# Performance work log

Hardware: AMD Instinct MI355X
Metric: run time of the kernel (lower is better)

## Reference

```python
import jax, jax.numpy as jnp
import numpy as np

N = 8192          # total nodes in the batch of graphs
ATOM = 64         # atom_feats
HID = 128         # hidden_feats
HEADS = 8         # num_heads
NUM_GRAPHS = 256  # number of graphs (max value of `batch`)
NEG_SLOPE = 0.2   # LeakyReLU slope in GAT attention


def setup_inputs() -> dict:
    key = jax.random.key(0)
    ks = jax.random.split(key, 16)
    x = jax.random.normal(ks[0], (N, ATOM), dtype=jnp.float32)
    adj = (jax.random.uniform(ks[1], (N, N)) < 0.01).astype(jnp.float32)
    adj = jnp.maximum(adj, jnp.eye(N, dtype=jnp.float32))
    batch = jnp.sort(jax.random.randint(ks[2], (N,), 0, NUM_GRAPHS)).astype(jnp.int32)

    def u(k, shape, fan_in):
        lim = 1.0 / np.sqrt(fan_in)
        return jax.random.uniform(k, shape, jnp.float32, -lim, lim)

    in1 = HID * HEADS
    params = dict(
        W0=u(ks[3], (ATOM, HID), ATOM), a0_src=u(ks[4], (HID,), HID), a0_dst=u(ks[5], (HID,), HID),
        W1=u(ks[6], (in1, HID), in1), a1_src=u(ks[7], (HID,), HID), a1_dst=u(ks[8], (HID,), HID),
        W2=u(ks[9], (in1, HID), in1), a2_src=u(ks[10], (HID,), HID), a2_dst=u(ks[11], (HID,), HID),
        fc_w=u(ks[12], (HID, 1), HID), fc_b=u(ks[13], (1,), HID),
    )
    return dict(x=x, adj=adj, batch=batch, **params)


def _gat_layer(h_in, W, a_src, a_dst, mask):
    # standard dense GAT: Wh, e_ij = leakyrelu(a_src.Wh_i + a_dst.Wh_j), masked softmax, aggregate
    h = h_in @ W                                         # [N, HID]
    e = jax.nn.leaky_relu((h @ a_src)[:, None] + (h @ a_dst)[None, :], NEG_SLOPE)  # [N, N]
    e = jnp.where(mask, e, jnp.float32(-1e9))
    attn = jax.nn.softmax(e, axis=1)                     # [N, N]
    return attn @ h                                      # [N, HID]


def reference(x, adj, batch, W0, a0_src, a0_dst, W1, a1_src, a1_dst, W2, a2_src, a2_dst, fc_w, fc_b):
    # eval mode: dropout is identity. The torch module calls the SAME layer instance per head,
    # so concat of heads == tile, and the final stacked mean == a single layer call.
    mask = adj > 0
    h0 = _gat_layer(x, W0, a0_src, a0_dst, mask)
    x1 = jax.nn.relu(jnp.tile(h0, (1, HEADS)))           # [N, HID*HEADS]
    h1 = _gat_layer(x1, W1, a1_src, a1_dst, mask)
    x2 = jax.nn.relu(jnp.tile(h1, (1, HEADS)))
    h2 = _gat_layer(x2, W2, a2_src, a2_dst, mask)        # mean over identical heads == h2
    # global mean pool over graphs
    sums = jax.ops.segment_sum(h2, batch, num_segments=NUM_GRAPHS)           # [G, HID]
    cnt = jax.ops.segment_sum(jnp.ones((N, 1), h2.dtype), batch, num_segments=NUM_GRAPHS)
    pooled = sums / jnp.maximum(cnt, 1.0)
    out = pooled @ fc_w + fc_b                           # [G, 1]
    return out[:, 0]
```

## Files before the change

### kernel.cpp

```cpp
#include <hip/hip_runtime.h>
#include <cstdint>
#include <cstddef>

#define NN 8192
#define ATOMF 64
#define HID 128
#define HEADS 8
#define NG 256
#define ELLW 192
#define NEGSLOPE 0.2f

typedef unsigned long long u64;

__global__ __launch_bounds__(256, 4) void k_scan_ell(const float* __restrict__ adj,
                                                     int* __restrict__ ell,
                                                     int* __restrict__ deg) {
    __shared__ u64 bml[4][128];
    int t = threadIdx.x, wid = t >> 6, l = t & 63;
    int row = blockIdx.x * 4 + wid;
    const float4* a4 = (const float4*)(adj + (size_t)row * NN);
    u64* bmr = bml[wid];
    #pragma unroll 8
    for (int s = 0; s < 32; ++s) {
        float4 v = a4[s * 64 + l];
        u64 b0 = __ballot(v.x > 0.f);
        u64 b1 = __ballot(v.y > 0.f);
        u64 b2 = __ballot(v.z > 0.f);
        u64 b3 = __ballot(v.w > 0.f);
        if (l < 4) bmr[s * 4 + l] = (l == 0) ? b0 : (l == 1) ? b1 : (l == 2) ? b2 : b3;
    }
    __syncthreads();
    u64 w0 = bmr[2 * l];
    u64 w1 = bmr[2 * l + 1];
    int c = __popcll(w0) + __popcll(w1);
    int incl = c;
    #pragma unroll
    for (int o = 1; o < 64; o <<= 1) {
        int u = __shfl_up(incl, o);
        if (l >= o) incl += u;
    }
    int pos = incl - c;
    int total = __shfl(incl, 63);
    if (l == 0) deg[row] = total < ELLW ? total : ELLW;
    int* er = ell + (size_t)row * ELLW;
    int gw0 = 2 * l, gw1 = 2 * l + 1;
    int base0 = (gw0 >> 2) * 256 + (gw0 & 3);
    int base1 = (gw1 >> 2) * 256 + (gw1 & 3);
    while (w0) {
        int bit = __builtin_ctzll(w0);
        w0 &= w0 - 1;
        if (pos < ELLW) er[pos++] = base0 + 4 * bit;
    }
    while (w1) {
        int bit = __builtin_ctzll(w1);
        w1 &= w1 - 1;
        if (pos < ELLW) er[pos++] = base1 + 4 * bit;
    }
}

__global__ __launch_bounds__(256) void k_front2(
    const float* __restrict__ x,
    const float* __restrict__ W0, const float* __restrict__ a0s, const float* __restrict__ a0d,
    const float* __restrict__ W1, const float* __restrict__ W2,
    float* __restrict__ Wr1, float* __restrict__ Wr2,
    float* __restrict__ g0, float* __restrict__ ssrc, float* __restrict__ sdst) {
    int b = blockIdx.x, t = threadIdx.x;
    if (b < 128) {
        const float* W = (b < 64) ? W1 : W2;
        float* Wr = (b < 64) ? Wr1 : Wr2;
        int i = (b & 63) * 256 + t;
        int k = i >> 7, cc = i & 127;
        float s = 0.f;
        #pragma unroll
        for (int h = 0; h < HEADS; ++h) s += W[(size_t)(h * HID + k) * HID + cc];
        Wr[i] = s;
    } else {
        __shared__ float Xl[32 * ATOMF];
        int row0 = (b - 128) * 32;
        const float4* Xg = (const float4*)(x + (size_t)row0 * ATOMF);
        float4* Xl4 = (float4*)Xl;
        #pragma unroll
        for (int i = t; i < 32 * ATOMF / 4; i += 256) Xl4[i] = Xg[i];
        __syncthreads();
        int cg = t & 31, rg = t >> 5;
        int c0 = cg * 4;
        float acc[4][4];
        #pragma unroll
        for (int r = 0; r < 4; ++r)
            #pragma unroll
            for (int c = 0; c < 4; ++c) acc[r][c] = 0.f;
        for (int k = 0; k < ATOMF; k += 4) {
            float4 w0 = *(const float4*)(W0 + (size_t)(k + 0) * HID + c0);
            float4 w1 = *(const float4*)(W0 + (size_t)(k + 1) * HID + c0);
            float4 w2 = *(const float4*)(W0 + (size_t)(k + 2) * HID + c0);
            float4 w3 = *(const float4*)(W0 + (size_t)(k + 3) * HID + c0);
            #pragma unroll
            for (int r = 0; r < 4; ++r) {
                float4 xv = *(const float4*)(&Xl[(rg * 4 + r) * ATOMF + k]);
                acc[r][0] += xv.x * w0.x + xv.y * w1.x + xv.z * w2.x + xv.w * w3.x;
                acc[r][1] += xv.x * w0.y + xv.y * w1.y + xv.z * w2.y + xv.w * w3.y;
                acc[r][2] += xv.x * w0.z + xv.y * w1.z + xv.z * w2.z + xv.w * w3.z;
                acc[r][3] += xv.x * w0.w + xv.y * w1.w + xv.z * w2.w + xv.w * w3.w;
            }
        }
        float4 asv = *(const float4*)(a0s + c0);
        float4 adv = *(const float4*)(a0d + c0);
        #pragma unroll
        for (int r = 0; r < 4; ++r) {
            int row = row0 + rg * 4 + r;
            *(float4*)(g0 + (size_t)row * HID + c0) =
                make_float4(acc[r][0], acc[r][1], acc[r][2], acc[r][3]);
            float ps = acc[r][0] * asv.x + acc[r][1] * asv.y + acc[r][2] * asv.z + acc[r][3] * asv.w;
            float pd = acc[r][0] * adv.x + acc[r][1] * adv.y + acc[r][2] * adv.z + acc[r][3] * adv.w;
            #pragma unroll
            for (int o = 16; o; o >>= 1) {
                ps += __shfl_xor(ps, o);
                pd += __shfl_xor(pd, o);
            }
            if (cg == 0) { ssrc[row] = ps; sdst[row] = pd; }
        }
    }
}

template<int DO_GEMM>
__global__ __launch_bounds__(256, 4) void k_layer(
    const float* __restrict__ g, const float* __restrict__ ssrc_in,
    const float* __restrict__ sdst_in,
    const int* __restrict__ ell, const int* __restrict__ deg,
    const float* __restrict__ Wr, const float* __restrict__ as_,
    const float* __restrict__ ad_,
    float* __restrict__ gout, float* __restrict__ ssrc_out,
    float* __restrict__ sdst_out) {
    __shared__ float wls[4][ELLW + 2];
    __shared__ int jls[4][ELLW + 2];
    __shared__ float xls[4][HID];
    int wid = threadIdx.x >> 6, l = threadIdx.x & 63;
    int row = blockIdx.x * 4 + wid;
    float* wl = wls[wid];
    int* jl = jls[wid];
    int d = deg[row];
    float si = ssrc_in[row];
    const int* er = ell + (size_t)row * ELLW;
    float m = -1e30f;
    for (int k = l; k < d; k += 64) {
        int j = er[k];
        float e = si + sdst_in[j];
        e = e > 0.f ? e : NEGSLOPE * e;
        jl[k] = j << 7;
        wl[k] = e;
        m = fmaxf(m, e);
    }
    #pragma unroll
    for (int o = 32; o; o >>= 1) m = fmaxf(m, __shfl_xor(m, o));
    float s = 0.f;
    for (int k = l; k < d; k += 64) {
        float w = __expf(wl[k] - m);
        wl[k] = w;
        s += w;
    }
    #pragma unroll
    for (int o = 32; o; o >>= 1) s += __shfl_xor(s, o);
    float inv = 1.f / s;
    if ((d & 1) && l == 0) { wl[d] = 0.f; jl[d] = 0; }
    int dpad = d + (d & 1);
    int half = l >> 5;
    int d0 = (l & 31) * 4;
    const float* hd = g + d0;
    float4 acc = make_float4(0.f, 0.f, 0.f, 0.f);
    int k = 0;
    for (; k + 8 <= dpad; k += 8) {
        int j0 = jl[k + half],     j1 = jl[k + 2 + half];
        int j2 = jl[k + 4 + half], j3 = jl[k + 6 + half];
        float w0 = wl[k + half],     w1 = wl[k + 2 + half];
        float w2 = wl[k + 4 + half], w3 = wl[k + 6 + half];
        float4 v0 = *(const float4*)(hd + j0);
        float4 v1 = *(const float4*)(hd + j1);
        float4 v2 = *(const float4*)(hd + j2);
        float4 v3 = *(const float4*)(hd + j3);
        acc.x += w0 * v0.x; acc.y += w0 * v0.y; acc.z += w0 * v0.z; acc.w += w0 * v0.w;
        acc.x += w1 * v1.x; acc.y += w1 * v1.y; acc.z += w1 * v1.z; acc.w += w1 * v1.w;
        acc.x += w2 * v2.x; acc.y += w2 * v2.y; acc.z += w2 * v2.z; acc.w += w2 * v2.w;
        acc.x += w3 * v3.x; acc.y += w3 * v3.y; acc.z += w3 * v3.z; acc.w += w3 * v3.w;
    }
    for (; k < dpad; k += 2) {
        int j = jl[k + half];
        float w = wl[k + half];
        float4 v = *(const float4*)(hd + j);
        acc.x += w * v.x; acc.y += w * v.y; acc.z += w * v.z; acc.w += w * v.w;
    }
    acc.x += __shfl_xor(acc.x, 32);
    acc.y += __shfl_xor(acc.y, 32);
    acc.z += __shfl_xor(acc.z, 32);
    acc.w += __shfl_xor(acc.w, 32);
    acc.x *= inv; acc.y *= inv; acc.z *= inv; acc.w *= inv;
    if (DO_GEMM == 0) {
        if (l < 32)
            *(float4*)(gout + (size_t)row * HID + d0) = acc;
        return;
    }
    float* xl = xls[wid];
    if (l < 32) {
        float4 r;
        r.x = fmaxf(acc.x, 0.f); r.y = fmaxf(acc.y, 0.f);
        r.z = fmaxf(acc.z, 0.f); r.w = fmaxf(acc.w, 0.f);
        *(float4*)(xl + d0) = r;
    }
    float acc0 = 0.f, acc1 = 0.f;
    for (int kk = 0; kk < HID; kk += 4) {
        float4 xv = *(const float4*)(&xl[kk]);
        float wa0 = Wr[(size_t)(kk + 0) * HID + l];
        float wb0 = Wr[(size_t)(kk + 0) * HID + l + 64];
        float wa1 = Wr[(size_t)(kk + 1) * HID + l];
        float wb1 = Wr[(size_t)(kk + 1) * HID + l + 64];
        float wa2 = Wr[(size_t)(kk + 2) * HID + l];
        float wb2 = Wr[(size_t)(kk + 2) * HID + l + 64];
        float wa3 = Wr[(size_t)(kk + 3) * HID + l];
        float wb3 = Wr[(size_t)(kk + 3) * HID + l + 64];
        acc0 += xv.x * wa0 + xv.y * wa1 + xv.z * wa2 + xv.w * wa3;
        acc1 += xv.x * wb0 + xv.y * wb1 + xv.z * wb2 + xv.w * wb3;
    }
    gout[(size_t)row * HID + l]      = acc0;
    gout[(size_t)row * HID + l + 64] = acc1;
    float ps = acc0 * as_[l] + acc1 * as_[l + 64];
    float pd = acc0 * ad_[l] + acc1 * ad_[l + 64];
    #pragma unroll
    for (int o = 32; o; o >>= 1) {
        ps += __shfl_xor(ps, o);
        pd += __shfl_xor(pd, o);
    }
    if (l == 0) { ssrc_out[row] = ps; sdst_out[row] = pd; }
}

__global__ __launch_bounds__(256) void k_poolfc(const float* __restrict__ h,
                                                const int* __restrict__ batch,
                                                const float* __restrict__ fcw,
                                                const float* __restrict__ fcb,
                                                float* __restrict__ out) {
    int wid = threadIdx.x >> 6, l = threadIdx.x & 63;
    int g = blockIdx.x * 4 + wid;
    int lo = 0, hi = NN;
    while (lo < hi) { int mid = (lo + hi) >> 1; if (batch[mid] < g) lo = mid + 1; else hi = mid; }
    int e0 = lo;
    hi = NN;
    while (lo < hi) { int mid = (lo + hi) >> 1; if (batch[mid] <= g) lo = mid + 1; else hi = mid; }
    int e1 = lo;
    float sum = 0.f;
    for (int r = e0; r < e1; ++r) {
        const float* hr = h + (size_t)r * HID;
        sum += hr[l] * fcw[l] + hr[l + 64] * fcw[l + 64];
    }
    #pragma unroll
    for (int o = 32; o; o >>= 1) sum += __shfl_xor(sum, o);
    if (l == 0) out[g] = sum / fmaxf((float)(e1 - e0), 1.f) + fcb[0];
}

extern "C" void kernel_launch(void* const* d_in, const int* in_sizes, int n_in,
                              void* d_out, int out_size, void* d_ws, size_t ws_size,
                              hipStream_t stream) {
    const float* x    = (const float*)d_in[0];
    const float* adj  = (const float*)d_in[1];
    const int*   batch= (const int*)  d_in[2];
    const float* W0   = (const float*)d_in[3];
    const float* a0s  = (const float*)d_in[4];
    const float* a0d  = (const float*)d_in[5];
    const float* W1   = (const float*)d_in[6];
    const float* a1s  = (const float*)d_in[7];
    const float* a1d  = (const float*)d_in[8];
    const float* W2   = (const float*)d_in[9];
    const float* a2s  = (const float*)d_in[10];
    const float* a2d  = (const float*)d_in[11];
    const float* fcw  = (const float*)d_in[12];
    const float* fcb  = (const float*)d_in[13];
    float* out = (float*)d_out;

    char* ws = (char*)d_ws;
    size_t off = 0;
    auto alloc = [&](size_t bytes) {
        char* p = ws + off;
        off = (off + bytes + 255) & ~255UL;
        return p;
    };
    int*   ell  = (int*)  alloc((size_t)NN * ELLW * 4);
    int*   deg  = (int*)  alloc((size_t)NN * 4);
    float* hA   = (float*)alloc((size_t)NN * HID * 4);
    float* hB   = (float*)alloc((size_t)NN * HID * 4);
    float* sAs  = (float*)alloc((size_t)NN * 4);
    float* sAd  = (float*)alloc((size_t)NN * 4);
    float* sBs  = (float*)alloc((size_t)NN * 4);
    float* sBd  = (float*)alloc((size_t)NN * 4);
    float* Wr1  = (float*)alloc((size_t)HID * HID * 4);
    float* Wr2  = (float*)alloc((size_t)HID * HID * 4);
    (void)ws_size; (void)in_sizes; (void)n_in; (void)out_size;

    k_scan_ell<<<NN / 4, 256, 0, stream>>>(adj, ell, deg);
    k_front2<<<128 + 256, 256, 0, stream>>>(x, W0, a0s, a0d, W1, W2,
                                            Wr1, Wr2, hA, sAs, sAd);
    k_layer<1><<<NN / 4, 256, 0, stream>>>(hA, sAs, sAd, ell, deg, Wr1, a1s, a1d,
                                           hB, sBs, sBd);
    k_layer<1><<<NN / 4, 256, 0, stream>>>(hB, sBs, sBd, ell, deg, Wr2, a2s, a2d,
                                           hA, sAs, sAd);
    k_layer<0><<<NN / 4, 256, 0, stream>>>(hA, sAs, sAd, ell, deg, nullptr, nullptr,
                                           nullptr, hB, nullptr, nullptr);
    k_poolfc<<<NG / 4, 256, 0, stream>>>(hB, batch, fcw, fcb, out);
}
```

Before: 171.1 us.

## Store node features in fp16 and drop softmax max-subtraction pass

Intermediate node feature matrices are now stored as fp16 to halve the bytes moved by the neighbor gather in each GAT layer. The per-row max reduction before the exponent is removed, so exp is computed directly in one pass. Degree is stored in an int4 record, and the GEMM weight loads are vectorised as float2. These changes risk lost precision and overflow in exp for large logits, but the main runtime is dominated by the adjacency scan, which is unchanged.

```diff
diff --git a/kernel.cpp b/kernel.cpp
--- a/kernel.cpp
+++ b/kernel.cpp
@@ -1,4 +1,5 @@
 #include <hip/hip_runtime.h>
+#include <hip/hip_fp16.h>
 #include <cstdint>
 #include <cstddef>
 
@@ -14,7 +15,7 @@
 
 __global__ __launch_bounds__(256, 4) void k_scan_ell(const float* __restrict__ adj,
                                                      int* __restrict__ ell,
-                                                     int* __restrict__ deg) {
+                                                     int4* __restrict__ tb) {
     __shared__ u64 bml[4][128];
     int t = threadIdx.x, wid = t >> 6, l = t & 63;
     int row = blockIdx.x * 4 + wid;
@@ -41,7 +42,12 @@
     }
     int pos = incl - c;
     int total = __shfl(incl, 63);
-    if (l == 0) deg[row] = total < ELLW ? total : ELLW;
+    if (l == 0) {
+        int4 b;
+        b.x = b.y = b.z = 0;
+        b.w = total < ELLW ? total : ELLW;
+        tb[row] = b;
+    }
     int* er = ell + (size_t)row * ELLW;
     int gw0 = 2 * l, gw1 = 2 * l + 1;
     int base0 = (gw0 >> 2) * 256 + (gw0 & 3);
@@ -63,7 +69,7 @@
     const float* __restrict__ W0, const float* __restrict__ a0s, const float* __restrict__ a0d,
     const float* __restrict__ W1, const float* __restrict__ W2,
     float* __restrict__ Wr1, float* __restrict__ Wr2,
-    float* __restrict__ g0, float* __restrict__ ssrc, float* __restrict__ sdst) {
+    __half* __restrict__ g016, float* __restrict__ ssrc, float* __restrict__ sdst) {
     int b = blockIdx.x, t = threadIdx.x;
     if (b < 128) {
         const float* W = (b < 64) ? W1 : W2;
@@ -108,8 +114,10 @@
         #pragma unroll
         for (int r = 0; r < 4; ++r) {
             int row = row0 + rg * 4 + r;
-            *(float4*)(g0 + (size_t)row * HID + c0) =
-                make_float4(acc[r][0], acc[r][1], acc[r][2], acc[r][3]);
+            __half2 p0 = __floats2half2_rn(acc[r][0], acc[r][1]);
+            __half2 p1 = __floats2half2_rn(acc[r][2], acc[r][3]);
+            __half2* gp = (__half2*)(g016 + (size_t)row * HID + c0);
+            gp[0] = p0; gp[1] = p1;
             float ps = acc[r][0] * asv.x + acc[r][1] * asv.y + acc[r][2] * asv.z + acc[r][3] * asv.w;
             float pd = acc[r][0] * adv.x + acc[r][1] * adv.y + acc[r][2] * adv.z + acc[r][3] * adv.w;
             #pragma unroll
@@ -124,37 +132,30 @@
 
 template<int DO_GEMM>
 __global__ __launch_bounds__(256, 4) void k_layer(
-    const float* __restrict__ g, const float* __restrict__ ssrc_in,
+    const __half* __restrict__ h16, const float* __restrict__ ssrc_in,
     const float* __restrict__ sdst_in,
-    const int* __restrict__ ell, const int* __restrict__ deg,
+    const int* __restrict__ ell, const int4* __restrict__ tb,
     const float* __restrict__ Wr, const float* __restrict__ as_,
     const float* __restrict__ ad_,
-    float* __restrict__ gout, float* __restrict__ ssrc_out,
-    float* __restrict__ sdst_out) {
+    __half* __restrict__ gout16, float* __restrict__ gout32,
+    float* __restrict__ ssrc_out, float* __restrict__ sdst_out) {
     __shared__ float wls[4][ELLW + 2];
-    __shared__ int jls[4][ELLW + 2];
+    __shared__ int   jls[4][ELLW + 2];
     __shared__ float xls[4][HID];
     int wid = threadIdx.x >> 6, l = threadIdx.x & 63;
     int row = blockIdx.x * 4 + wid;
     float* wl = wls[wid];
     int* jl = jls[wid];
-    int d = deg[row];
+    int d = tb[row].w;
     float si = ssrc_in[row];
     const int* er = ell + (size_t)row * ELLW;
-    float m = -1e30f;
+    float s = 0.f;
     for (int k = l; k < d; k += 64) {
         int j = er[k];
         float e = si + sdst_in[j];
         e = e > 0.f ? e : NEGSLOPE * e;
+        float w = __expf(e);
         jl[k] = j << 7;
-        wl[k] = e;
-        m = fmaxf(m, e);
-    }
-    #pragma unroll
-    for (int o = 32; o; o >>= 1) m = fmaxf(m, __shfl_xor(m, o));
-    float s = 0.f;
-    for (int k = l; k < d; k += 64) {
-        float w = __expf(wl[k] - m);
         wl[k] = w;
         s += w;
     }
@@ -165,7 +166,7 @@
     int dpad = d + (d & 1);
     int half = l >> 5;
     int d0 = (l & 31) * 4;
-    const float* hd = g + d0;
+    const __half* hd = h16 + d0;
     float4 acc = make_float4(0.f, 0.f, 0.f, 0.f);
     int k = 0;
     for (; k + 8 <= dpad; k += 8) {
@@ -173,20 +174,25 @@
         int j2 = jl[k + 4 + half], j3 = jl[k + 6 + half];
         float w0 = wl[k + half],     w1 = wl[k + 2 + half];
         float w2 = wl[k + 4 + half], w3 = wl[k + 6 + half];
-        float4 v0 = *(const float4*)(hd + j0);
-        float4 v1 = *(const float4*)(hd + j1);
-        float4 v2 = *(const float4*)(hd + j2);
-        float4 v3 = *(const float4*)(hd + j3);
-        acc.x += w0 * v0.x; acc.y += w0 * v0.y; acc.z += w0 * v0.z; acc.w += w0 * v0.w;
-        acc.x += w1 * v1.x; acc.y += w1 * v1.y; acc.z += w1 * v1.z; acc.w += w1 * v1.w;
-        acc.x += w2 * v2.x; acc.y += w2 * v2.y; acc.z += w2 * v2.z; acc.w += w2 * v2.w;
-        acc.x += w3 * v3.x; acc.y += w3 * v3.y; acc.z += w3 * v3.z; acc.w += w3 * v3.w;
+        int2 r0 = *(const int2*)(hd + j0);
+        int2 r1 = *(const int2*)(hd + j1);
+        int2 r2 = *(const int2*)(hd + j2);
+        int2 r3 = *(const int2*)(hd + j3);
+        float2 a0 = __half22float2(*(__half2*)&r0.x), b0 = __half22float2(*(__half2*)&r0.y);
+        float2 a1 = __half22float2(*(__half2*)&r1.x), b1 = __half22float2(*(__half2*)&r1.y);
+        float2 a2 = __half22float2(*(__half2*)&r2.x), b2 = __half22float2(*(__half2*)&r2.y);
+        float2 a3 = __half22float2(*(__half2*)&r3.x), b3 = __half22float2(*(__half2*)&r3.y);
+        acc.x += w0 * a0.x; acc.y += w0 * a0.y; acc.z += w0 * b0.x; acc.w += w0 * b0.y;
+        acc.x += w1 * a1.x; acc.y += w1 * a1.y; acc.z += w1 * b1.x; acc.w += w1 * b1.y;
+        acc.x += w2 * a2.x; acc.y += w2 * a2.y; acc.z += w2 * b2.x; acc.w += w2 * b2.y;
+        acc.x += w3 * a3.x; acc.y += w3 * a3.y; acc.z += w3 * b3.x; acc.w += w3 * b3.y;
     }
     for (; k < dpad; k += 2) {
         int j = jl[k + half];
         float w = wl[k + half];
-        float4 v = *(const float4*)(hd + j);
-        acc.x += w * v.x; acc.y += w * v.y; acc.z += w * v.z; acc.w += w * v.w;
+        int2 r0 = *(const int2*)(hd + j);
+        float2 a0 = __half22float2(*(__half2*)&r0.x), b0 = __half22float2(*(__half2*)&r0.y);
+        acc.x += w * a0.x; acc.y += w * a0.y; acc.z += w * b0.x; acc.w += w * b0.y;
     }
     acc.x += __shfl_xor(acc.x, 32);
     acc.y += __shfl_xor(acc.y, 32);
@@ -195,7 +201,7 @@
     acc.x *= inv; acc.y *= inv; acc.z *= inv; acc.w *= inv;
     if (DO_GEMM == 0) {
         if (l < 32)
-            *(float4*)(gout + (size_t)row * HID + d0) = acc;
+            *(float4*)(gout32 + (size_t)row * HID + d0) = acc;
         return;
     }
     float* xl = xls[wid];
@@ -205,24 +211,22 @@
         r.z = fmaxf(acc.z, 0.f); r.w = fmaxf(acc.w, 0.f);
         *(float4*)(xl + d0) = r;
     }
+    int c2 = 2 * l;
     float acc0 = 0.f, acc1 = 0.f;
     for (int kk = 0; kk < HID; kk += 4) {
         float4 xv = *(const float4*)(&xl[kk]);
-        float wa0 = Wr[(size_t)(kk + 0) * HID + l];
-        float wb0 = Wr[(size_t)(kk + 0) * HID + l + 64];
-        float wa1 = Wr[(size_t)(kk + 1) * HID + l];
-        float wb1 = Wr[(size_t)(kk + 1) * HID + l + 64];
-        float wa2 = Wr[(size_t)(kk + 2) * HID + l];
-        float wb2 = Wr[(size_t)(kk + 2) * HID + l + 64];
-        float wa3 = Wr[(size_t)(kk + 3) * HID + l];
-        float wb3 = Wr[(size_t)(kk + 3) * HID + l + 64];
-        acc0 += xv.x * wa0 + xv.y * wa1 + xv.z * wa2 + xv.w * wa3;
-        acc1 += xv.x * wb0 + xv.y * wb1 + xv.z * wb2 + xv.w * wb3;
-    }
-    gout[(size_t)row * HID + l]      = acc0;
-    gout[(size_t)row * HID + l + 64] = acc1;
-    float ps = acc0 * as_[l] + acc1 * as_[l + 64];
-    float pd = acc0 * ad_[l] + acc1 * ad_[l + 64];
+        float2 w0 = *(const float2*)(Wr + (size_t)(kk + 0) * HID + c2);
+        float2 w1 = *(const float2*)(Wr + (size_t)(kk + 1) * HID + c2);
+        float2 w2 = *(const float2*)(Wr + (size_t)(kk + 2) * HID + c2);
+        float2 w3 = *(const float2*)(Wr + (size_t)(kk + 3) * HID + c2);
+        acc0 += xv.x * w0.x + xv.y * w1.x + xv.z * w2.x + xv.w * w3.x;
+        acc1 += xv.x * w0.y + xv.y * w1.y + xv.z * w2.y + xv.w * w3.y;
+    }
+    *(__half2*)(gout16 + (size_t)row * HID + c2) = __floats2half2_rn(acc0, acc1);
+    float2 asv = *(const float2*)(as_ + c2);
+    float2 adv = *(const float2*)(ad_ + c2);
+    float ps = acc0 * asv.x + acc1 * asv.y;
+    float pd = acc0 * adv.x + acc1 * adv.y;
     #pragma unroll
     for (int o = 32; o; o >>= 1) {
         ps += __shfl_xor(ps, o);
@@ -280,26 +284,27 @@
         off = (off + bytes + 255) & ~255UL;
         return p;
     };
-    int*   ell  = (int*)  alloc((size_t)NN * ELLW * 4);
-    int*   deg  = (int*)  alloc((size_t)NN * 4);
-    float* hA   = (float*)alloc((size_t)NN * HID * 4);
-    float* hB   = (float*)alloc((size_t)NN * HID * 4);
-    float* sAs  = (float*)alloc((size_t)NN * 4);
-    float* sAd  = (float*)alloc((size_t)NN * 4);
-    float* sBs  = (float*)alloc((size_t)NN * 4);
-    float* sBd  = (float*)alloc((size_t)NN * 4);
-    float* Wr1  = (float*)alloc((size_t)HID * HID * 4);
-    float* Wr2  = (float*)alloc((size_t)HID * HID * 4);
+    int*    ell  = (int*)   alloc((size_t)NN * ELLW * 4);
+    int4*   tb   = (int4*)  alloc((size_t)NN * 16);
+    __half* hA16 = (__half*)alloc((size_t)NN * HID * 2);
+    __half* hB16 = (__half*)alloc((size_t)NN * HID * 2);
+    float*  h2   = (float*) alloc((size_t)NN * HID * 4);
+    float*  sAs  = (float*) alloc((size_t)NN * 4);
+    float*  sAd  = (float*) alloc((size_t)NN * 4);
+    float*  sBs  = (float*) alloc((size_t)NN * 4);
+    float*  sBd  = (float*) alloc((size_t)NN * 4);
+    float*  Wr1  = (float*) alloc((size_t)HID * HID * 4);
+    float*  Wr2  = (float*) alloc((size_t)HID * HID * 4);
     (void)ws_size; (void)in_sizes; (void)n_in; (void)out_size;
 
-    k_scan_ell<<<NN / 4, 256, 0, stream>>>(adj, ell, deg);
+    k_scan_ell<<<NN / 4, 256, 0, stream>>>(adj, ell, tb);
     k_front2<<<128 + 256, 256, 0, stream>>>(x, W0, a0s, a0d, W1, W2,
-                                            Wr1, Wr2, hA, sAs, sAd);
-    k_layer<1><<<NN / 4, 256, 0, stream>>>(hA, sAs, sAd, ell, deg, Wr1, a1s, a1d,
-                                           hB, sBs, sBd);
-    k_layer<1><<<NN / 4, 256, 0, stream>>>(hB, sBs, sBd, ell, deg, Wr2, a2s, a2d,
-                                           hA, sAs, sAd);
-    k_layer<0><<<NN / 4, 256, 0, stream>>>(hA, sAs, sAd, ell, deg, nullptr, nullptr,
-                                           nullptr, hB, nullptr, nullptr);
-    k_poolfc<<<NG / 4, 256, 0, stream>>>(hB, batch, fcw, fcb, out);
-}
+                                            Wr1, Wr2, hA16, sAs, sAd);
+    k_layer<1><<<NN / 4, 256, 0, stream>>>(hA16, sAs, sAd, ell, tb, Wr1, a1s, a1d,
+                                           hB16, nullptr, sBs, sBd);
+    k_layer<1><<<NN / 4, 256, 0, stream>>>(hB16, sBs, sBd, ell, tb, Wr2, a2s, a2d,
+                                           hA16, nullptr, sAs, sAd);
+    k_layer<0><<<NN / 4, 256, 0, stream>>>(hA16, sAs, sAd, ell, tb, nullptr, nullptr,
+                                           nullptr, nullptr, h2, nullptr, nullptr);
+    k_poolfc<<<NG / 4, 256, 0, stream>>>(h2, batch, fcw, fcb, out);
+}
```

Result: slower. 183.0 us (+7.0%).
